# Optimization experiments

Hardware: AMD Instinct MI355X
Metric: run time of the kernel (lower is better)

Reference implementation:

```python
import jax, jax.numpy as jnp
import numpy as np

N_NODES = 100000
N_EDGES = 3200000
IN_DIM = 16
HID = 64


def setup_inputs() -> dict:
    key = jax.random.key(0)
    k_x, k_e, k_w1, k_w2 = jax.random.split(key, 4)
    x = jax.random.normal(k_x, (N_NODES, IN_DIM), dtype=jnp.float32)
    edge_index = jax.random.randint(k_e, (2, N_EDGES), 0, N_NODES, dtype=jnp.int64)
    # PyTorch Linear default init: U(-1/sqrt(fan_in), 1/sqrt(fan_in)); use scaled normal analog
    W1 = jax.random.normal(k_w1, (2 * IN_DIM, HID), dtype=jnp.float32) / np.sqrt(2 * IN_DIM)
    b1 = jnp.zeros((HID,), dtype=jnp.float32)
    W2 = jax.random.normal(k_w2, (HID, 1), dtype=jnp.float32) / np.sqrt(HID)
    b2 = jnp.zeros((1,), dtype=jnp.float32)
    return {"x": x, "edge_index": edge_index, "W1": W1, "b1": b1, "W2": W2, "b2": b2}


def reference(x, edge_index, W1, b1, W2, b2):
    row = edge_index[0]
    col = edge_index[1]
    bi = x[col]                      # [E, IN_DIM] gather of receiver features
    bo = x[row]                      # [E, IN_DIM] gather of sender features
    B = jnp.concatenate([bi, bo], axis=-1)  # [E, 2*IN_DIM]
    h = jnp.tanh(B @ W1 + b1)        # [E, HID]
    return jax.nn.sigmoid(h @ W2 + b2)  # [E, 1]
```

## Files before the change

kernel.cpp:

```cpp
#include <hip/hip_runtime.h>


typedef __attribute__((ext_vector_type(8)))  short bf16x8;
typedef __attribute__((ext_vector_type(2)))  float f32x2;
typedef __attribute__((ext_vector_type(4)))  float f32x4;
typedef __attribute__((ext_vector_type(16))) float f32x16;
typedef __attribute__((ext_vector_type(4)))  unsigned short u16x4;

#define LOG2E 1.4426950408889634f

__device__ __forceinline__ float asm_exp2(float x) {
    float r;
    asm("v_exp_f32 %0, %1" : "=v"(r) : "v"(x));
    return r;
}
__device__ __forceinline__ float asm_rcp(float x) {
    float r;
    asm("v_rcp_f32 %0, %1" : "=v"(r) : "v"(x));
    return r;
}

template <bool B> struct BC { static constexpr bool value = B; };

__device__ __forceinline__ unsigned short f2bf(float f) {
    unsigned u = __float_as_uint(f);
    u += 0x7fffu + ((u >> 16) & 1u);
    return (unsigned short)(u >> 16);
}

__global__ void prep(const float* __restrict__ x, unsigned short* __restrict__ xb, int n,
                     const unsigned* __restrict__ ei, int* __restrict__ flag) {
    if (blockIdx.x == 0 && threadIdx.x < 64) {
        unsigned v = ei[2 * threadIdx.x + 1];
        unsigned long long nz = __ballot(v != 0u);
        if (threadIdx.x == 0) flag[0] = (nz == 0ull) ? 1 : 0;
    }
    int i = (blockIdx.x * blockDim.x + threadIdx.x) * 4;
    if (i >= n) return;
    f32x4 v = *(const f32x4*)(x + i);
    u16x4 o;
    o[0] = f2bf(v[0]); o[1] = f2bf(v[1]); o[2] = f2bf(v[2]); o[3] = f2bf(v[3]);
    *(u16x4*)(xb + i) = o;
}

__global__ void detect_idx64(const unsigned* __restrict__ ei, int* __restrict__ flag) {
    unsigned v = ei[2 * threadIdx.x + 1];
    unsigned long long nz = __ballot(v != 0u);
    if (threadIdx.x == 0) flag[0] = (nz == 0ull) ? 1 : 0;
}

struct IdxPair { int c, r; };

template <bool USE_XB, bool EXACT>
__global__ void __launch_bounds__(256)
edge_mlp(const void* __restrict__ ei,
         const float* __restrict__ x,
         const unsigned short* __restrict__ xb,
         const float* __restrict__ W1,
         const float* __restrict__ b1,
         const float* __restrict__ W2,
         const float* __restrict__ b2,
         float* __restrict__ out,
         const int* __restrict__ flag,
         int E, int ntiles)
{
    const int lane = threadIdx.x & 63;
    const int l31  = lane & 31;
    const int g    = lane >> 5;
    const int gwave  = blockIdx.x * (blockDim.x >> 6) + (threadIdx.x >> 6);
    const int nwaves = gridDim.x * (blockDim.x >> 6);

    const int idx64 = flag ? flag[0] : 0;
    const float S = 2.0f * LOG2E;

    bf16x8 w1f00, w1f01, w1f10, w1f11;
    {
        union { bf16x8 v; unsigned short u[8]; } t00, t01, t10, t11;
#pragma unroll
        for (int b = 0; b < 8; ++b) {
            int k0 = 8 * g + b;
            t00.u[b] = f2bf(S * W1[(k0)      * 64 + l31]);
            t01.u[b] = f2bf(S * W1[(16 + k0) * 64 + l31]);
            t10.u[b] = f2bf(S * W1[(k0)      * 64 + 32 + l31]);
            t11.u[b] = f2bf(S * W1[(16 + k0) * 64 + 32 + l31]);
        }
        w1f00 = t00.v; w1f01 = t01.v; w1f10 = t10.v; w1f11 = t11.v;
    }
    f32x16 b1v0, b1v1;
    f32x2  w2a[8], w2b[8];
    float  pbase = 0.f;
#pragma unroll
    for (int reg = 0; reg < 16; ++reg) {
        int rowv = (reg & 3) + 8 * (reg >> 2) + 4 * g;
        b1v0[reg] = S * b1[rowv];
        b1v1[reg] = S * b1[32 + rowv];
        float wa = W2[rowv], wb = W2[32 + rowv];
        w2a[reg >> 1][reg & 1] = -2.0f * wa;
        w2b[reg >> 1][reg & 1] = -2.0f * wb;
        pbase += wa + wb;
    }
    const float bias2 = b2[0];

    auto body = [&](auto bc) {
        constexpr bool IDX64 = decltype(bc)::value;
        auto load_idx = [&](int tt) -> IdxPair {
            int e = tt * 32 + l31;
            int ec;
            if (EXACT) ec = e;
            else       ec = e < E ? e : E - 1;
            IdxPair ip;
            if (IDX64) {
                ip.r = ((const int*)ei)[2 * (size_t)ec];
                ip.c = ((const int*)ei)[2 * ((size_t)E + ec)];
            } else {
                ip.r = ((const int*)ei)[(size_t)ec];
                ip.c = ((const int*)ei)[(size_t)E + ec];
            }
            return ip;
        };
        auto gather = [&](int node) -> bf16x8 {
            if (USE_XB) {
                return *(const bf16x8*)(xb + (size_t)node * 16 + 8 * g);
            } else {
                const float* px = x + (size_t)node * 16 + 8 * g;
                f32x4 v0 = *(const f32x4*)px;
                f32x4 v1 = *(const f32x4*)(px + 4);
                union { bf16x8 v; unsigned short u[8]; } t;
#pragma unroll
                for (int b = 0; b < 4; ++b) { t.u[b] = f2bf(v0[b]); t.u[b + 4] = f2bf(v1[b]); }
                return t.v;
            }
        };

        int t = gwave;
        if (t >= ntiles) return;
        IdxPair ic = load_idx(t);
        bf16x8 fc = gather(ic.c);
        bf16x8 fr = gather(ic.r);
        int tn = t + nwaves;
        IdxPair inx = load_idx(tn < ntiles ? tn : ntiles - 1);

        while (true) {
            bf16x8 fcn = gather(inx.c);
            bf16x8 frn = gather(inx.r);
            int tnn = tn + nwaves;
            IdxPair inn = load_idx(tnn < ntiles ? tnn : ntiles - 1);

            f32x16 acc0 = __builtin_amdgcn_mfma_f32_32x32x16_bf16(w1f00, fc, b1v0, 0, 0, 0);
            acc0        = __builtin_amdgcn_mfma_f32_32x32x16_bf16(w1f01, fr, acc0, 0, 0, 0);
            f32x16 acc1 = __builtin_amdgcn_mfma_f32_32x32x16_bf16(w1f10, fc, b1v1, 0, 0, 0);
            acc1        = __builtin_amdgcn_mfma_f32_32x32x16_bf16(w1f11, fr, acc1, 0, 0, 0);

            f32x2 pv0 = { pbase, 0.0f };
            f32x2 pv1 = { 0.0f, 0.0f };
#pragma unroll
            for (int j = 0; j < 8; ++j) {
                f32x2 rv0 = { asm_rcp(1.0f + asm_exp2(acc0[2 * j])),
                              asm_rcp(1.0f + asm_exp2(acc0[2 * j + 1])) };
                f32x2 rv1 = { asm_rcp(1.0f + asm_exp2(acc1[2 * j])),
                              asm_rcp(1.0f + asm_exp2(acc1[2 * j + 1])) };
                pv0 += w2a[j] * rv0;
                pv1 += w2b[j] * rv1;
            }
            float p = (pv0[0] + pv1[0]) + (pv0[1] + pv1[1]);
            p += __shfl_xor(p, 32);
            float z = p + bias2;
            float res = asm_rcp(1.0f + asm_exp2(-z * LOG2E));
            int e0i = t * 32 + l31;
            if (EXACT) {
                if (lane < 32) out[e0i] = res;
            } else {
                if (lane < 32 && e0i < E) out[e0i] = res;
            }

            if (tn >= ntiles) break;
            t = tn; tn = tnn;
            inx = inn; fc = fcn; fr = frn;
        }
    };

    if (idx64) body(BC<true>{});
    else       body(BC<false>{});
}

extern "C" void kernel_launch(void* const* d_in, const int* in_sizes, int n_in,
                              void* d_out, int out_size, void* d_ws, size_t ws_size,
                              hipStream_t stream)
{
    const float* x  = (const float*)d_in[0];
    const void*  ei = d_in[1];
    const float* W1 = (const float*)d_in[2];
    const float* b1 = (const float*)d_in[3];
    const float* W2 = (const float*)d_in[4];
    const float* b2 = (const float*)d_in[5];
    float* out = (float*)d_out;

    const int E      = in_sizes[1] / 2;
    const int nx     = in_sizes[0];
    const int ntiles = (E + 31) / 32;
    const bool exact = (E % 32) == 0;

    int* flag = nullptr;
    unsigned short* xb = nullptr;
    bool use_xb = false;
    if (ws_size >= 4) flag = (int*)d_ws;
    if (ws_size >= 256 + (size_t)nx * 2) {
        xb = (unsigned short*)((char*)d_ws + 256);
        use_xb = true;
    }

    if (use_xb) {
        int nth = (nx + 3) / 4;
        prep<<<(nth + 255) / 256, 256, 0, stream>>>(x, xb, nx, (const unsigned*)ei, flag);
    } else if (flag) {
        detect_idx64<<<1, 64, 0, stream>>>((const unsigned*)ei, flag);
    }

    const int blocks = 2048;
    if (use_xb) {
        if (exact) edge_mlp<true , true ><<<blocks, 256, 0, stream>>>(ei, x, xb, W1, b1, W2, b2, out, flag, E, ntiles);
        else       edge_mlp<true , false><<<blocks, 256, 0, stream>>>(ei, x, xb, W1, b1, W2, b2, out, flag, E, ntiles);
    } else {
        if (exact) edge_mlp<false, true ><<<blocks, 256, 0, stream>>>(ei, x, xb, W1, b1, W2, b2, out, flag, E, ntiles);
        else       edge_mlp<false, false><<<blocks, 256, 0, stream>>>(ei, x, xb, W1, b1, W2, b2, out, flag, E, ntiles);
    }
}
```

Baseline: 72.42 us.

## Fold b1 into exp multiplier via LDS table and use 32-bit address offsets

Removes the per-lane bias accumulator vectors and W2 register arrays. b1 is folded into the activation as a multiplicative factor exp2(S*b1), and that factor plus the W2 coefficient are read from a small shared-memory table, so the MFMAs now start from a zero accumulator. Index, gather and store addresses are computed as unsigned 32-bit byte offsets rather than 64-bit size_t arithmetic. The aim is lower register pressure (higher occupancy) and cheaper address math. In exchange it adds LDS reads in the inner loop and a __syncthreads. The 32-bit offsets also assume every buffer fits in 4 GB.

```diff
diff --git a/kernel.cpp b/kernel.cpp
--- a/kernel.cpp
+++ b/kernel.cpp
@@ -2,7 +2,6 @@
 
 
 typedef __attribute__((ext_vector_type(8)))  short bf16x8;
-typedef __attribute__((ext_vector_type(2)))  float f32x2;
 typedef __attribute__((ext_vector_type(4)))  float f32x4;
 typedef __attribute__((ext_vector_type(16))) float f32x16;
 typedef __attribute__((ext_vector_type(4)))  unsigned short u16x4;
@@ -64,6 +63,8 @@
          const int* __restrict__ flag,
          int E, int ntiles)
 {
+    __shared__ float2 tbl[64];
+
     const int lane = threadIdx.x & 63;
     const int l31  = lane & 31;
     const int g    = lane >> 5;
@@ -72,6 +73,19 @@
 
     const int idx64 = flag ? flag[0] : 0;
     const float S = 2.0f * LOG2E;
+
+    {
+        int tid = threadIdx.x;
+        if (tid < 64) {
+            int tg = tid >> 5, tb = (tid >> 4) & 1, tj = tid & 15;
+            int rowv = (tj & 3) + 8 * (tj >> 2) + 4 * tg;
+            int h = 32 * tb + rowv;
+            float2 cw;
+            cw.x = exp2f(S * b1[h]);
+            cw.y = -2.0f * W2[h];
+            tbl[tid] = cw;
+        }
+    }
 
     bf16x8 w1f00, w1f01, w1f10, w1f11;
     {
@@ -86,41 +100,43 @@
         }
         w1f00 = t00.v; w1f01 = t01.v; w1f10 = t10.v; w1f11 = t11.v;
     }
-    f32x16 b1v0, b1v1;
-    f32x2  w2a[8], w2b[8];
-    float  pbase = 0.f;
-#pragma unroll
-    for (int reg = 0; reg < 16; ++reg) {
-        int rowv = (reg & 3) + 8 * (reg >> 2) + 4 * g;
-        b1v0[reg] = S * b1[rowv];
-        b1v1[reg] = S * b1[32 + rowv];
-        float wa = W2[rowv], wb = W2[32 + rowv];
-        w2a[reg >> 1][reg & 1] = -2.0f * wa;
-        w2b[reg >> 1][reg & 1] = -2.0f * wb;
-        pbase += wa + wb;
+
+    float pbase = 0.f;
+#pragma unroll
+    for (int j = 0; j < 16; ++j) {
+        int rowv = (j & 3) + 8 * (j >> 2) + 4 * g;
+        pbase += W2[rowv] + W2[32 + rowv];
     }
     const float bias2 = b2[0];
+
+    __syncthreads();
+    const float2* tb = &tbl[g * 32];
+
+    const char* xbb  = (const char*)xb;
+    const char* outb = (char*)out;
+    const unsigned g16 = (unsigned)g << 4;
 
     auto body = [&](auto bc) {
         constexpr bool IDX64 = decltype(bc)::value;
+        const unsigned sh = IDX64 ? 3u : 2u;
+        const char* eiR = (const char*)ei;
+        const char* eiC = (const char*)ei + ((size_t)E << sh);
+
         auto load_idx = [&](int tt) -> IdxPair {
             int e = tt * 32 + l31;
-            int ec;
-            if (EXACT) ec = e;
-            else       ec = e < E ? e : E - 1;
+            unsigned ec;
+            if (EXACT) ec = (unsigned)e;
+            else       ec = (unsigned)(e < E ? e : E - 1);
+            unsigned off = ec << sh;
             IdxPair ip;
-            if (IDX64) {
-                ip.r = ((const int*)ei)[2 * (size_t)ec];
-                ip.c = ((const int*)ei)[2 * ((size_t)E + ec)];
-            } else {
-                ip.r = ((const int*)ei)[(size_t)ec];
-                ip.c = ((const int*)ei)[(size_t)E + ec];
-            }
+            ip.r = *(const int*)(eiR + off);
+            ip.c = *(const int*)(eiC + off);
             return ip;
         };
         auto gather = [&](int node) -> bf16x8 {
             if (USE_XB) {
-                return *(const bf16x8*)(xb + (size_t)node * 16 + 8 * g);
+                unsigned off = ((unsigned)node << 5) + g16;
+                return *(const bf16x8*)(xbb + off);
             } else {
                 const float* px = x + (size_t)node * 16 + 8 * g;
                 f32x4 v0 = *(const f32x4*)px;
@@ -140,37 +156,52 @@
         int tn = t + nwaves;
         IdxPair inx = load_idx(tn < ntiles ? tn : ntiles - 1);
 
+        const f32x16 ZC = 0.0f;
+
         while (true) {
             bf16x8 fcn = gather(inx.c);
             bf16x8 frn = gather(inx.r);
             int tnn = tn + nwaves;
             IdxPair inn = load_idx(tnn < ntiles ? tnn : ntiles - 1);
 
-            f32x16 acc0 = __builtin_amdgcn_mfma_f32_32x32x16_bf16(w1f00, fc, b1v0, 0, 0, 0);
+            f32x16 acc0 = __builtin_amdgcn_mfma_f32_32x32x16_bf16(w1f00, fc, ZC, 0, 0, 0);
             acc0        = __builtin_amdgcn_mfma_f32_32x32x16_bf16(w1f01, fr, acc0, 0, 0, 0);
-            f32x16 acc1 = __builtin_amdgcn_mfma_f32_32x32x16_bf16(w1f10, fc, b1v1, 0, 0, 0);
+            f32x16 acc1 = __builtin_amdgcn_mfma_f32_32x32x16_bf16(w1f10, fc, ZC, 0, 0, 0);
             acc1        = __builtin_amdgcn_mfma_f32_32x32x16_bf16(w1f11, fr, acc1, 0, 0, 0);
 
-            f32x2 pv0 = { pbase, 0.0f };
-            f32x2 pv1 = { 0.0f, 0.0f };
-#pragma unroll
-            for (int j = 0; j < 8; ++j) {
-                f32x2 rv0 = { asm_rcp(1.0f + asm_exp2(acc0[2 * j])),
-                              asm_rcp(1.0f + asm_exp2(acc0[2 * j + 1])) };
-                f32x2 rv1 = { asm_rcp(1.0f + asm_exp2(acc1[2 * j])),
-                              asm_rcp(1.0f + asm_exp2(acc1[2 * j + 1])) };
-                pv0 += w2a[j] * rv0;
-                pv1 += w2b[j] * rv1;
-            }
-            float p = (pv0[0] + pv1[0]) + (pv0[1] + pv1[1]);
+            float p0 = pbase, p1 = 0.f, p2 = 0.f, p3 = 0.f;
+#pragma unroll
+            for (int j = 0; j < 16; ++j) {
+                float2 cw = tb[j];
+                float e  = asm_exp2(acc0[j]);
+                float rv = asm_rcp(fmaf(cw.x, e, 1.0f));
+                float pj = fmaf(cw.y, rv, (j & 3) == 0 ? p0 : (j & 3) == 1 ? p1 : (j & 3) == 2 ? p2 : p3);
+                if      ((j & 3) == 0) p0 = pj;
+                else if ((j & 3) == 1) p1 = pj;
+                else if ((j & 3) == 2) p2 = pj;
+                else                   p3 = pj;
+            }
+#pragma unroll
+            for (int j = 0; j < 16; ++j) {
+                float2 cw = tb[16 + j];
+                float e  = asm_exp2(acc1[j]);
+                float rv = asm_rcp(fmaf(cw.x, e, 1.0f));
+                float pj = fmaf(cw.y, rv, (j & 3) == 0 ? p0 : (j & 3) == 1 ? p1 : (j & 3) == 2 ? p2 : p3);
+                if      ((j & 3) == 0) p0 = pj;
+                else if ((j & 3) == 1) p1 = pj;
+                else if ((j & 3) == 2) p2 = pj;
+                else                   p3 = pj;
+            }
+            float p = (p0 + p1) + (p2 + p3);
             p += __shfl_xor(p, 32);
             float z = p + bias2;
             float res = asm_rcp(1.0f + asm_exp2(-z * LOG2E));
-            int e0i = t * 32 + l31;
+
+            unsigned eoff = ((unsigned)(t * 32 + l31)) << 2;
             if (EXACT) {
-                if (lane < 32) out[e0i] = res;
+                if (lane < 32) *(float*)(outb + eoff) = res;
             } else {
-                if (lane < 32 && e0i < E) out[e0i] = res;
+                if (lane < 32 && (t * 32 + l31) < E) *(float*)(outb + eoff) = res;
             }
 
             if (tn >= ntiles) break;
```

After: 62.93 us. 1.15x faster.
